# Performance work log

Measured on AMD Instinct MI355X. Metric: run time of the kernel, lower is better.

## Reference

```python
import jax, jax.numpy as jnp
import numpy as np

BSZ = 4
SL = 4096
NPAD = 8192  # next power of two >= 2*SL (preconvolve)
K = 16       # num_eigh
D = 128      # n_embd
KU = 3       # k_u
NM = 2       # num_models (residual boosting)
NL = 2       # n_layers per SpectralSSM
DIN = 64     # vocab / d_in
DOUT = 64    # d_out
HID = 512    # scale * n_embd
EPS = 1e-6


def _top_eigh(sl, k):
    # Hankel matrix Z[i,j] = 2 / ((i+j)^3 - (i+j)), 1-indexed
    idx = np.arange(1, sl + 1, dtype=np.float64)
    s = idx[:, None] + idx[None, :]
    Z = 2.0 / (s ** 3 - s)
    w, v = np.linalg.eigh(Z)
    return np.abs(w[-k:]).astype(np.float32), v[:, -k:].astype(np.float32)


def setup_inputs() -> dict:
    key = jax.random.key(0)
    ks = jax.random.split(key, 12)
    sigma_np, phi_np = _top_eigh(SL, K)
    mx = DOUT ** (-0.5)
    std = 0.02
    return {
        "inputs": jax.random.randint(ks[0], (BSZ, SL), 0, DIN),
        "targets": jax.random.randint(ks[1], (BSZ, SL), 0, DOUT),
        "sigma": jnp.asarray(sigma_np),
        "phi": jnp.asarray(phi_np),
        "embed_w": std * jax.random.normal(ks[2], (NM, DIN, D), jnp.float32),
        "rn_w": jnp.ones((NM, NL, D), jnp.float32),
        "M_u": jax.random.uniform(ks[3], (NM, NL, KU, D, D), jnp.float32, -mx, mx),
        "M_phi_plus": std * jax.random.normal(ks[4], (NM, NL, K, D, D), jnp.float32),
        "M_phi_minus": std * jax.random.normal(ks[5], (NM, NL, K, D, D), jnp.float32),
        "fc1_w": std * jax.random.normal(ks[6], (NM, NL, 2 * HID, D), jnp.float32),
        "fc2_w": std * jax.random.normal(ks[7], (NM, NL, D, HID), jnp.float32),
        "out_w": std * jax.random.normal(ks[8], (NM, DOUT, D), jnp.float32),
    }


def _rms(x, w):
    return x * jax.lax.rsqrt(jnp.mean(x * x, axis=-1, keepdims=True) + EPS) * w


def _mlp(x, w1, w2):
    h = x @ w1.T                      # (b, s, 2*HID)
    y, gate = h[..., :HID], h[..., HID:]
    return (y * jax.nn.silu(gate)) @ w2.T


def _stu(x, V, alt, Mp, Mm, Mu):
    # spectral FFT long convolution with K eigenfilters
    U = jnp.fft.rfft(x, n=NPAD, axis=1)                                   # (b, F, d)
    Up = jnp.fft.irfft(V[None, :, :, None] * U[:, :, None, :], n=NPAD, axis=1)[:, :SL]  # (b, s, K, d)
    Ua = jnp.fft.rfft(x * alt[None, :, None], n=NPAD, axis=1)
    Um = jnp.fft.irfft(V[None, :, :, None] * Ua[:, :, None, :], n=NPAD, axis=1)[:, :SL]
    y = jnp.einsum('bski,kio->bso', Up, Mp) + jnp.einsum('bski,kio->bso', Um, Mm)
    ar = jnp.einsum('bsd,do->bso', x, Mu[0])
    for i in range(1, KU):
        xs = jnp.pad(x, ((0, 0), (i, 0), (0, 0)))[:, :SL]
        ar = ar + jnp.einsum('bsd,do->bso', xs, Mu[i])
    return y + ar


def reference(inputs, targets, sigma, phi, embed_w, rn_w, M_u, M_phi_plus,
              M_phi_minus, fc1_w, fc2_w, out_w):
    phi_s = phi * sigma[None, :] ** 0.25                 # fold sigma^{1/4} into filters
    V = jnp.fft.rfft(phi_s, n=NPAD, axis=0)              # (F, K), preconvolve
    alt = ((-1.0) ** jnp.arange(SL)).astype(phi.dtype)

    residual = jax.nn.one_hot(targets, DOUT, dtype=phi.dtype)
    total = None
    for m in range(NM):
        x = embed_w[m][inputs]                           # (b, s, d)
        for l in range(NL):
            z = x
            x = x + _stu(_rms(x, rn_w[m, l]), V, alt,
                         M_phi_plus[m, l], M_phi_minus[m, l], M_u[m, l])
            x = x + _mlp(x, fc1_w[m, l], fc2_w[m, l])
            x = x + z
        logits = x @ out_w[m].T                          # (b, s, DOUT)
        total = logits if total is None else total + logits
        residual = residual - jax.lax.stop_gradient(logits)  # boosting target for next model
    return total
```

## Files before the change

kernel.cpp:

```cpp
#include <hip/hip_runtime.h>
#include <hip/hip_bf16.h>
#include <cstdint>

typedef unsigned short u16;
typedef __attribute__((ext_vector_type(8))) short bf16x8;
typedef __attribute__((ext_vector_type(4))) float f32x4;

#define N_ROWS 16384

__device__ __forceinline__ float bf2f(u16 u){ union{unsigned i; float f;} v; v.i = ((unsigned)u)<<16; return v.f; }
__device__ __forceinline__ u16 f2bf(float f){ union{float f; unsigned i;} v; v.f = f; unsigned r = v.i + 0x7fffu + ((v.i>>16)&1u); return (u16)(r>>16); }

__device__ __forceinline__ void gl2lds(const u16* g, u16* l){
  __builtin_amdgcn_global_load_lds((const __attribute__((address_space(1))) void*)g,
                                   (__attribute__((address_space(3))) void*)l, 16, 0, 0);
}


__global__ __launch_bounds__(256) void buildT_k(const float* __restrict__ phi, const float* __restrict__ sigma,
                                                u16* __restrict__ T){
  int idx = blockIdx.x*256 + threadIdx.x;
  int t2 = idx & 63;
  int tt = (idx>>6) & 127;
  int o  = (idx>>13) & 31;
  int k  = idx>>18;
  float sp = powf(sigma[k], 0.25f);
  int d0 = o*128 + tt - t2*2;
  float v0 = (d0   >= 0) ? phi[(size_t)d0*16 + k]*sp     : 0.f;
  float v1 = (d0-1 >= 0) ? phi[(size_t)(d0-1)*16 + k]*sp : 0.f;
  ushort2 u; u.x = f2bf(v0); u.y = f2bf(v1);
  ((ushort2*)T)[idx] = u;
}

__global__ __launch_bounds__(256) void castw_k(const float* __restrict__ Mp, const float* __restrict__ Mm,
                                               u16* __restrict__ W){
  int z = blockIdx.z; int ml = z>>5, k = (z>>1)&15, pm = z&1;
  const float* src = (pm ? Mm : Mp) + (size_t)(ml*16 + k)*16384;
  u16* dst = W + (size_t)ml*(2048*256) + (size_t)(k*128)*256 + pm*128;
  __shared__ float t[32][33];
  int ty = threadIdx.x>>5, tx = threadIdx.x&31;
  int i0 = blockIdx.x*32, o0 = blockIdx.y*32;
#pragma unroll
  for (int j=0;j<4;++j) t[ty+j*8][tx] = src[(size_t)(i0+ty+j*8)*128 + o0+tx];
  __syncthreads();
#pragma unroll
  for (int j=0;j<4;++j){
    int o = o0 + ty + j*8, i = i0 + tx;
    dst[(size_t)o*256 + i] = f2bf(t[tx][ty+j*8]);
  }
}

__global__ __launch_bounds__(256) void castmu_k(const float* __restrict__ Mu, u16* __restrict__ MuT){
  int z = blockIdx.z; int ml = z/3, j = z%3;
  const float* src = Mu + (size_t)(ml*3 + j)*16384;
  u16* dst = MuT + (size_t)ml*(128*384) + j*128;
  __shared__ float t[32][33];
  int ty = threadIdx.x>>5, tx = threadIdx.x&31;
  int i0 = blockIdx.x*32, o0 = blockIdx.y*32;
#pragma unroll
  for (int jj=0;jj<4;++jj) t[ty+jj*8][tx] = src[(size_t)(i0+ty+jj*8)*128 + o0+tx];
  __syncthreads();
#pragma unroll
  for (int jj=0;jj<4;++jj){
    int o = o0 + ty + jj*8, i = i0 + tx;
    dst[(size_t)o*384 + i] = f2bf(t[tx][ty+jj*8]);
  }
}

__global__ __launch_bounds__(256) void castf_k(const float* __restrict__ src, u16* __restrict__ dst, int n4){
  int i = blockIdx.x*256 + threadIdx.x;
  if (i < n4){
    float4 v = ((const float4*)src)[i];
    ushort4 u; u.x=f2bf(v.x); u.y=f2bf(v.y); u.z=f2bf(v.z); u.w=f2bf(v.w);
    ((ushort4*)dst)[i] = u;
  }
}


__global__ __launch_bounds__(256) void embed_k(const int* __restrict__ tok, const float* __restrict__ E,
                                               float* __restrict__ x){
  int idx = blockIdx.x*256 + threadIdx.x;
  int r = idx>>5, q = idx&31;
  int t = tok[r];
  ((float4*)(x + (size_t)r*128))[q] = ((const float4*)(E + (size_t)t*128))[q];
}

__global__ __launch_bounds__(256) void rms_k(const float* __restrict__ x, const float* __restrict__ w,
                                             u16* __restrict__ Xcat){
  int wave = threadIdx.x>>6, lane = threadIdx.x&63;
  int r = blockIdx.x*4 + wave;
  float2 xv = ((const float2*)(x + (size_t)r*128))[lane];
  float ss = xv.x*xv.x + xv.y*xv.y;
  for (int off=32; off; off>>=1) ss += __shfl_xor(ss, off, 64);
  float sc = rsqrtf(ss*(1.f/128.f) + 1e-6f);
  float2 wv = ((const float2*)w)[lane];
  float a = xv.x*sc*wv.x, b = xv.y*sc*wv.y;
  int s = r & 4095;
  float sg = (s & 1) ? -1.f : 1.f;
  ushort2* row = (ushort2*)(Xcat + (size_t)r*256);
  ushort2 u0; u0.x = f2bf(a);    u0.y = f2bf(b);
  ushort2 u1; u1.x = f2bf(a*sg); u1.y = f2bf(b*sg);
  row[lane]      = u0;
  row[64 + lane] = u1;
}

__global__ __launch_bounds__(256) void xar_k(const u16* __restrict__ Xcat, u16* __restrict__ Xar){
  int idx = blockIdx.x*256 + threadIdx.x;
  int r = idx>>5, q4 = idx&31;
  int s = r & 4095;
  ushort4 z; z.x=0; z.y=0; z.z=0; z.w=0;
#pragma unroll
  for (int j=0;j<3;++j){
    ushort4 v = (s >= j) ? ((const ushort4*)Xcat)[(size_t)(r-j)*64 + q4] : z;
    ((ushort4*)Xar)[(size_t)r*96 + j*32 + q4] = v;
  }
}

__global__ __launch_bounds__(256) void mid_k(const float* __restrict__ x, const float* __restrict__ Y,
                                             const u16* __restrict__ Yp, float* __restrict__ xmid,
                                             u16* __restrict__ xmbf){
  size_t idx = (size_t)blockIdx.x*256 + threadIdx.x;
  float4 xv = ((const float4*)x)[idx];
  float4 a  = ((const float4*)Y)[idx];
  const size_t P = (size_t)N_ROWS*32;
#pragma unroll
  for (int g=0; g<16; ++g){
    ushort4 v = ((const ushort4*)Yp)[idx + (size_t)g*P];
    a.x += bf2f(v.x); a.y += bf2f(v.y); a.z += bf2f(v.z); a.w += bf2f(v.w);
  }
  float4 r; r.x = xv.x+a.x; r.y = xv.y+a.y; r.z = xv.z+a.z; r.w = xv.w+a.w;
  ((float4*)xmid)[idx] = r;
  ushort4 u; u.x=f2bf(r.x); u.y=f2bf(r.y); u.z=f2bf(r.z); u.w=f2bf(r.w);
  ((ushort4*)xmbf)[idx] = u;
}

__global__ __launch_bounds__(256) void gate_k(const u16* __restrict__ h, u16* __restrict__ hg){
  size_t idx = (size_t)blockIdx.x*256 + threadIdx.x;
  size_t r = idx>>7, c = idx&127;
  ushort4 yv = ((const ushort4*)(h + r*1024))[c];
  ushort4 gv = ((const ushort4*)(h + r*1024 + 512))[c];
  float g0=bf2f(gv.x), g1=bf2f(gv.y), g2=bf2f(gv.z), g3=bf2f(gv.w);
  float s0 = g0/(1.f+expf(-g0)), s1 = g1/(1.f+expf(-g1)), s2 = g2/(1.f+expf(-g2)), s3 = g3/(1.f+expf(-g3));
  ushort4 o;
  o.x = f2bf(bf2f(yv.x)*s0); o.y = f2bf(bf2f(yv.y)*s1);
  o.z = f2bf(bf2f(yv.z)*s2); o.w = f2bf(bf2f(yv.w)*s3);
  ((ushort4*)(hg + r*512))[c] = o;
}

__global__ __launch_bounds__(256) void logits_k(const float* __restrict__ x, const u16* __restrict__ Wt,
                                                float* __restrict__ out, int accum){
  __shared__ u16 lw[64*130];
  for (int i = threadIdx.x; i < 8192; i += 256) lw[(i>>7)*130 + (i&127)] = Wt[i];
  __syncthreads();
  int wave = threadIdx.x>>6, lane = threadIdx.x&63;
  int r = blockIdx.x*4 + wave;
  const float* xr = x + (size_t)r*128;
  float acc = 0.f;
#pragma unroll
  for (int i=0;i<128;i+=4){
    float4 xv = *(const float4*)&xr[i];
    acc += xv.x*bf2f(lw[lane*130+i  ]) + xv.y*bf2f(lw[lane*130+i+1])
         + xv.z*bf2f(lw[lane*130+i+2]) + xv.w*bf2f(lw[lane*130+i+3]);
  }
  size_t o = (size_t)r*64 + lane;
  out[o] = accum ? (out[o] + acc) : acc;
}

template<int EPI>
__global__ __launch_bounds__(256) void gemm_k(const u16* __restrict__ A, int lda,
    const u16* __restrict__ Bt, int ldb, int Kdim, int ldc,
    u16* __restrict__ obf, float* __restrict__ of32,
    const float* __restrict__ e1, float* __restrict__ e2)
{
  __shared__ u16 Al[128*64];
  __shared__ u16 Bl[128*64];
  const int tid = threadIdx.x, w = tid>>6, lane = tid&63;
  const int wr = w>>1, wc = w&1;
  const int r0 = blockIdx.x*128, c0 = blockIdx.y*128;
  const int ccs = (((lane&7) ^ (lane>>3)))*8;
  f32x4 acc[4][4] = {};
  for (int k0 = 0; k0 < Kdim; k0 += 64){
#pragma unroll
    for (int i=0;i<4;++i){
      const int rr = w*32 + i*8 + (lane>>3);
      gl2lds(A  + (size_t)(r0+rr)*lda + k0 + ccs, &Al[(w*32+i*8)*64]);
      gl2lds(Bt + (size_t)(c0+rr)*ldb + k0 + ccs, &Bl[(w*32+i*8)*64]);
    }
    __syncthreads();
#pragma unroll
    for (int ks=0; ks<2; ++ks){
      const int rc = (((ks*4 + (lane>>4)) ^ (lane&7)))*8;
      bf16x8 av[4], bv[4];
#pragma unroll
      for (int mi=0;mi<4;++mi) av[mi] = *(const bf16x8*)&Al[(wr*64+mi*16+(lane&15))*64 + rc];
#pragma unroll
      for (int ni=0;ni<4;++ni) bv[ni] = *(const bf16x8*)&Bl[(wc*64+ni*16+(lane&15))*64 + rc];
#pragma unroll
      for (int mi=0;mi<4;++mi)
#pragma unroll
        for (int ni=0;ni<4;++ni)
          acc[mi][ni] = __builtin_amdgcn_mfma_f32_16x16x32_bf16(av[mi], bv[ni], acc[mi][ni], 0,0,0);
    }
    __syncthreads();
  }
  const int lr = (lane>>4)*4, lc = lane&15;
#pragma unroll
  for (int mi=0;mi<4;++mi){
#pragma unroll
    for (int ni=0;ni<4;++ni){
      const int gr = r0 + wr*64 + mi*16 + lr;
      const int gc = c0 + wc*64 + ni*16 + lc;
      if (EPI == 0){
#pragma unroll
        for (int j=0;j<4;++j) of32[(size_t)(gr+j)*ldc + gc] = acc[mi][ni][j];
      } else if (EPI == 1){
#pragma unroll
        for (int j=0;j<4;++j) obf[(size_t)(gr+j)*ldc + gc] = f2bf(acc[mi][ni][j]);
      } else if (EPI == 2){
        ushort4 u; u.x=f2bf(acc[mi][ni][0]); u.y=f2bf(acc[mi][ni][1]);
                   u.z=f2bf(acc[mi][ni][2]); u.w=f2bf(acc[mi][ni][3]);
        const int bb = gr>>12, tau = gr&4095;
        *(ushort4*)&obf[((size_t)(bb*2048 + gc))*4096 + tau] = u;
      } else {
#pragma unroll
        for (int j=0;j<4;++j){ const size_t id = (size_t)(gr+j)*ldc + gc; e2[id] = acc[mi][ni][j] + e1[id] + e2[id]; }
      }
    }
  }
}

__global__ __launch_bounds__(256) void timemix_k(const u16* __restrict__ T, const u16* __restrict__ G,
                                                 u16* __restrict__ Yp)
{
  __shared__ u16 Al[128*64];
  __shared__ u16 Bl[128*64];
  const int bid = blockIdx.x;
  const int k  = bid & 15;
  const int b  = (bid>>4) & 3;
  const int qq = bid>>6;
  const int tid = threadIdx.x, w = tid>>6, lane = tid&63;
  const int wr = w>>1, wc = w&1;
  const int ccs = (((lane&7) ^ (lane>>3)))*8;
  const u16* Tk = T + (size_t)k*32*16384;
  const u16* Gk = G + ((size_t)(b*2048 + k*128))*4096;
  u16* o = Yp + (size_t)k*((size_t)N_ROWS*128) + (size_t)b*4096*128;
  const int lr = (lane>>4)*4, lc = lane&15;
  for (int qi = 0; qi < 2; ++qi){
    const int q = qi ? (31-qq) : qq;
    f32x4 acc[4][4] = {};
    for (int p = 0; p <= q; ++p){
      const u16* Ab = Tk + (size_t)(q-p)*16384;
      const u16* Bb = Gk + (size_t)p*128;
#pragma unroll
      for (int hh=0; hh<2; ++hh){
        const int k0 = hh*64;
#pragma unroll
        for (int i=0;i<4;++i){
          const int rr = w*32 + i*8 + (lane>>3);
          gl2lds(Ab + (size_t)rr*128  + k0 + ccs, &Al[(w*32+i*8)*64]);
          gl2lds(Bb + (size_t)rr*4096 + k0 + ccs, &Bl[(w*32+i*8)*64]);
        }
        __syncthreads();
#pragma unroll
        for (int ks=0; ks<2; ++ks){
          const int rc = (((ks*4 + (lane>>4)) ^ (lane&7)))*8;
          bf16x8 av[4], bv[4];
#pragma unroll
          for (int mi=0;mi<4;++mi) av[mi] = *(const bf16x8*)&Al[(wr*64+mi*16+(lane&15))*64 + rc];
#pragma unroll
          for (int ni=0;ni<4;++ni) bv[ni] = *(const bf16x8*)&Bl[(wc*64+ni*16+(lane&15))*64 + rc];
#pragma unroll
          for (int mi=0;mi<4;++mi)
#pragma unroll
            for (int ni=0;ni<4;++ni)
              acc[mi][ni] = __builtin_amdgcn_mfma_f32_16x16x32_bf16(av[mi], bv[ni], acc[mi][ni], 0,0,0);
        }
        __syncthreads();
      }
    }
#pragma unroll
    for (int mi=0;mi<4;++mi){
#pragma unroll
      for (int ni=0;ni<4;++ni){
        const int grl = q*128 + wr*64 + mi*16 + lr;
        const int gc  = wc*64 + ni*16 + lc;
#pragma unroll
        for (int j=0;j<4;++j) o[(size_t)(grl + j)*128 + gc] = f2bf(acc[mi][ni][j]);
      }
    }
  }
}

extern "C" void kernel_launch(void* const* d_in, const int* in_sizes, int n_in,
                              void* d_out, int out_size, void* d_ws, size_t ws_size,
                              hipStream_t stream)
{
  const int*   inputs = (const int*)d_in[0];
  const float* sigma  = (const float*)d_in[2];
  const float* phi    = (const float*)d_in[3];
  const float* embed  = (const float*)d_in[4];
  const float* rnw    = (const float*)d_in[5];
  const float* Mu     = (const float*)d_in[6];
  const float* Mp     = (const float*)d_in[7];
  const float* Mm     = (const float*)d_in[8];
  const float* fc1    = (const float*)d_in[9];
  const float* fc2    = (const float*)d_in[10];
  const float* outw   = (const float*)d_in[11];
  float* out = (float*)d_out;
  char* ws = (char*)d_ws;
  size_t off = 0;
  auto alloc = [&](size_t b){ size_t o = off; off += (b + 255) & ~(size_t)255; return o; };
  u16*   T    = (u16*)  (ws + alloc((size_t)16*32*16384*2));
  u16*   Wcat = (u16*)  (ws + alloc((size_t)4*2048*256*2));
  u16*   MuT  = (u16*)  (ws + alloc((size_t)4*128*384*2));
  u16*   f1T  = (u16*)  (ws + alloc((size_t)524288*2));
  u16*   f2T  = (u16*)  (ws + alloc((size_t)262144*2));
  u16*   owT  = (u16*)  (ws + alloc((size_t)16384*2));
  float* x    = (float*)(ws + alloc((size_t)N_ROWS*128*4));
  float* Y    = (float*)(ws + alloc((size_t)N_ROWS*128*4));
  u16*   Ypb  = (u16*)  (ws + alloc((size_t)16*N_ROWS*128*2));
  float* xmid = (float*)(ws + alloc((size_t)N_ROWS*128*4));
  u16*   xmbf = (u16*)  (ws + alloc((size_t)N_ROWS*128*2));
  u16*   big  = (u16*)  (ws + alloc((size_t)N_ROWS*2048*2));
  u16*   Xar  = Ypb;
  u16*   Xcat = Ypb + (size_t)N_ROWS*384;
  u16*   Gt = big;
  u16*   h  = big;
  u16*   hg = big + (size_t)N_ROWS*1024;

  buildT_k <<<16384, 256, 0, stream>>>(phi, sigma, T);
  castw_k  <<<dim3(4,4,128), 256, 0, stream>>>(Mp, Mm, Wcat);
  castmu_k <<<dim3(4,4,12),  256, 0, stream>>>(Mu, MuT);
  castf_k  <<<512, 256, 0, stream>>>(fc1,  f1T, 131072);
  castf_k  <<<256, 256, 0, stream>>>(fc2,  f2T, 65536);
  castf_k  <<<16,  256, 0, stream>>>(outw, owT, 4096);

  for (int m = 0; m < 2; ++m){
    embed_k<<<2048, 256, 0, stream>>>(inputs, embed + (size_t)m*8192, x);
    for (int l = 0; l < 2; ++l){
      const int ml = m*2 + l;
      rms_k<<<4096, 256, 0, stream>>>(x, rnw + ml*128, Xcat);
      xar_k<<<2048, 256, 0, stream>>>(Xcat, Xar);
      gemm_k<0><<<dim3(128,1), 256, 0, stream>>>(Xar, 384, MuT + (size_t)ml*128*384, 384, 384, 128,
                                                 nullptr, Y, nullptr, nullptr);
      gemm_k<2><<<dim3(128,16), 256, 0, stream>>>(Xcat, 256, Wcat + (size_t)ml*2048*256, 256, 256, 0,
                                                  Gt, nullptr, nullptr, nullptr);
      timemix_k<<<1024, 256, 0, stream>>>(T, Gt, Ypb);
      mid_k<<<2048, 256, 0, stream>>>(x, Y, Ypb, xmid, xmbf);
      gemm_k<1><<<dim3(128,8), 256, 0, stream>>>(xmbf, 128, f1T + (size_t)ml*1024*128, 128, 128, 1024,
                                                 h, nullptr, nullptr, nullptr);
      gate_k<<<8192, 256, 0, stream>>>(h, hg);
      gemm_k<3><<<dim3(128,1), 256, 0, stream>>>(hg, 512, f2T + (size_t)ml*128*512, 512, 512, 128,
                                                 nullptr, nullptr, xmid, x);
    }
    logits_k<<<4096, 256, 0, stream>>>(x, owT + (size_t)m*8192, out, m);
  }
}
```

Before: 1.250 ms.

## Restructure timemix into 256-row tiles with triple-buffered async LDS pipeline

The Toeplitz time-mixing GEMM now uses 512-thread blocks computing 256-row output tiles, with each block accumulating two eigenfilters into one partial output. This halves the partial buffers that mid_k must sum. The T matrix gains an extra zero-padded diagonal block so that 256-row tiles can index it uniformly. The inner loop uses a three-stage LDS ring with direct global-to-LDS loads, explicit vmcnt waits, raw barriers and setprio around the MFMAs, so that loads overlap compute. The cost is more LDS per block, fewer blocks, and fragile hand-placed waits.

```diff
diff --git a/kernel.cpp b/kernel.cpp
--- a/kernel.cpp
+++ b/kernel.cpp
@@ -22,10 +22,11 @@
   int idx = blockIdx.x*256 + threadIdx.x;
   int t2 = idx & 63;
   int tt = (idx>>6) & 127;
-  int o  = (idx>>13) & 31;
-  int k  = idx>>18;
+  unsigned rest = ((unsigned)idx)>>13;
+  int k  = rest / 33u;
+  int oi = rest - 33u*k;
   float sp = powf(sigma[k], 0.25f);
-  int d0 = o*128 + tt - t2*2;
+  int d0 = (oi-1)*128 + tt - t2*2;
   float v0 = (d0   >= 0) ? phi[(size_t)d0*16 + k]*sp     : 0.f;
   float v1 = (d0-1 >= 0) ? phi[(size_t)(d0-1)*16 + k]*sp : 0.f;
   ushort2 u; u.x = f2bf(v0); u.y = f2bf(v1);
@@ -124,7 +125,7 @@
   float4 a  = ((const float4*)Y)[idx];
   const size_t P = (size_t)N_ROWS*32;
 #pragma unroll
-  for (int g=0; g<16; ++g){
+  for (int g=0; g<8; ++g){
     ushort4 v = ((const ushort4*)Yp)[idx + (size_t)g*P];
     a.x += bf2f(v.x); a.y += bf2f(v.y); a.z += bf2f(v.z); a.w += bf2f(v.w);
   }
@@ -229,63 +230,110 @@
   }
 }
 
-__global__ __launch_bounds__(256) void timemix_k(const u16* __restrict__ T, const u16* __restrict__ G,
-                                                 u16* __restrict__ Yp)
+__global__ __launch_bounds__(512, 2) void timemix_k(const u16* __restrict__ T, const u16* __restrict__ G,
+                                                    u16* __restrict__ Yp)
 {
-  __shared__ u16 Al[128*64];
-  __shared__ u16 Bl[128*64];
+  __shared__ u16 Al[3][256*64];
+  __shared__ u16 Bl[3][128*64];
   const int bid = blockIdx.x;
-  const int k  = bid & 15;
-  const int b  = (bid>>4) & 3;
-  const int qq = bid>>6;
+  const int kg = bid & 7;
+  const int b  = (bid>>3) & 3;
+  const int pj = bid>>5;
   const int tid = threadIdx.x, w = tid>>6, lane = tid&63;
   const int wr = w>>1, wc = w&1;
-  const int ccs = (((lane&7) ^ (lane>>3)))*8;
-  const u16* Tk = T + (size_t)k*32*16384;
-  const u16* Gk = G + ((size_t)(b*2048 + k*128))*4096;
-  u16* o = Yp + (size_t)k*((size_t)N_ROWS*128) + (size_t)b*4096*128;
+  const int l8 = lane>>3;
+  const int ccs = ((lane&7) ^ l8)*8;
+  const int fr = lane&15;
+  const int frx = lane&7;
   const int lr = (lane>>4)*4, lc = lane&15;
-  for (int qi = 0; qi < 2; ++qi){
-    const int q = qi ? (31-qq) : qq;
+  const int rc0 = (((lane>>4)    ) ^ frx)*8;
+  const int rc1 = (((lane>>4) + 4) ^ frx)*8;
+  u16* oYp = Yp + (size_t)kg*((size_t)N_ROWS*128) + (size_t)b*4096*128;
+
+  for (int sp = 0; sp < 2; ++sp){
+    const int jq = sp ? (15-pj) : pj;
+    const int NT = 4*jq + 4;
+    const int TT = 2*NT;
+
+    auto stage = [&](int t, int part, int sbuf){
+      int tk = t, kk = kg*2;
+      if (tk >= NT){ tk -= NT; kk++; }
+      const int p = tk>>1, k0 = (tk&1)*64;
+      const u16* Tk = T + (size_t)kk*33*16384;
+      const u16* Gk = G + ((size_t)(b*2048 + kk*128))*4096 + (size_t)p*128 + k0 + ccs;
+      u16* Ab = Al[sbuf]; u16* Bb = Bl[sbuf];
+#pragma unroll
+      for (int i = part*2; i < part*2+2; ++i){
+        const int rr = w*32 + i*8;
+        const int offI = 2*jq + (rr>>7) - p + 1;
+        gl2lds(Tk + (size_t)offI*16384 + (size_t)((rr&127)+l8)*128 + k0 + ccs, &Ab[rr*64]);
+      }
+      const int ro = w*16 + part*8;
+      gl2lds(Gk + (size_t)(ro+l8)*4096, &Bb[ro*64]);
+    };
+
+    stage(0,0,0); stage(0,1,0);
+    stage(1,0,1); stage(1,1,1);
+    asm volatile("s_waitcnt vmcnt(6)");
+    __builtin_amdgcn_s_barrier();
+
     f32x4 acc[4][4] = {};
-    for (int p = 0; p <= q; ++p){
-      const u16* Ab = Tk + (size_t)(q-p)*16384;
-      const u16* Bb = Gk + (size_t)p*128;
-#pragma unroll
-      for (int hh=0; hh<2; ++hh){
-        const int k0 = hh*64;
-#pragma unroll
-        for (int i=0;i<4;++i){
-          const int rr = w*32 + i*8 + (lane>>3);
-          gl2lds(Ab + (size_t)rr*128  + k0 + ccs, &Al[(w*32+i*8)*64]);
-          gl2lds(Bb + (size_t)rr*4096 + k0 + ccs, &Bl[(w*32+i*8)*64]);
+    int cur = 0;
+    for (int t = 0; t < TT; ++t){
+      const int sbuf = (cur+2 >= 3) ? cur-1 : cur+2;
+      const u16* Ab = Al[cur]; const u16* Bb = Bl[cur];
+      {
+        bf16x8 av[4], bv[4];
+#pragma unroll
+        for (int mi=0;mi<4;++mi) av[mi] = *(const bf16x8*)&Ab[(wr*64+mi*16+fr)*64 + rc0];
+#pragma unroll
+        for (int ni=0;ni<4;++ni) bv[ni] = *(const bf16x8*)&Bb[(wc*64+ni*16+fr)*64 + rc0];
+        if (t+2 < TT) stage(t+2, 0, sbuf);
+        __builtin_amdgcn_s_barrier();
+        asm volatile("s_waitcnt lgkmcnt(0)");
+        __builtin_amdgcn_sched_barrier(0);
+        __builtin_amdgcn_s_setprio(1);
+#pragma unroll
+        for (int mi=0;mi<4;++mi)
+#pragma unroll
+          for (int ni=0;ni<4;++ni)
+            acc[mi][ni] = __builtin_amdgcn_mfma_f32_16x16x32_bf16(av[mi], bv[ni], acc[mi][ni], 0,0,0);
+        __builtin_amdgcn_s_setprio(0);
+        __builtin_amdgcn_s_barrier();
+      }
+      {
+        bf16x8 av[4], bv[4];
+#pragma unroll
+        for (int mi=0;mi<4;++mi) av[mi] = *(const bf16x8*)&Ab[(wr*64+mi*16+fr)*64 + rc1];
+#pragma unroll
+        for (int ni=0;ni<4;++ni) bv[ni] = *(const bf16x8*)&Bb[(wc*64+ni*16+fr)*64 + rc1];
+        if (t+2 < TT) stage(t+2, 1, sbuf);
+        __builtin_amdgcn_s_barrier();
+        asm volatile("s_waitcnt lgkmcnt(0)");
+        __builtin_amdgcn_sched_barrier(0);
+        __builtin_amdgcn_s_setprio(1);
+#pragma unroll
+        for (int mi=0;mi<4;++mi)
+#pragma unroll
+          for (int ni=0;ni<4;++ni)
+            acc[mi][ni] = __builtin_amdgcn_mfma_f32_16x16x32_bf16(av[mi], bv[ni], acc[mi][ni], 0,0,0);
+        __builtin_amdgcn_s_setprio(0);
+        if (t+1 < TT){
+          if (t+2 < TT) asm volatile("s_waitcnt vmcnt(6)");
+          else          asm volatile("s_waitcnt vmcnt(0)");
         }
-        __syncthreads();
-#pragma unroll
-        for (int ks=0; ks<2; ++ks){
-          const int rc = (((ks*4 + (lane>>4)) ^ (lane&7)))*8;
-          bf16x8 av[4], bv[4];
-#pragma unroll
-          for (int mi=0;mi<4;++mi) av[mi] = *(const bf16x8*)&Al[(wr*64+mi*16+(lane&15))*64 + rc];
-#pragma unroll
-          for (int ni=0;ni<4;++ni) bv[ni] = *(const bf16x8*)&Bl[(wc*64+ni*16+(lane&15))*64 + rc];
-#pragma unroll
-          for (int mi=0;mi<4;++mi)
-#pragma unroll
-            for (int ni=0;ni<4;++ni)
-              acc[mi][ni] = __builtin_amdgcn_mfma_f32_16x16x32_bf16(av[mi], bv[ni], acc[mi][ni], 0,0,0);
-        }
-        __syncthreads();
+        __builtin_amdgcn_s_barrier();
       }
+      cur = (cur==2) ? 0 : cur+1;
     }
 #pragma unroll
     for (int mi=0;mi<4;++mi){
 #pragma unroll
       for (int ni=0;ni<4;++ni){
-        const int grl = q*128 + wr*64 + mi*16 + lr;
+        const int grl = jq*256 + wr*64 + mi*16 + lr;
         const int gc  = wc*64 + ni*16 + lc;
 #pragma unroll
-        for (int j=0;j<4;++j) o[(size_t)(grl + j)*128 + gc] = f2bf(acc[mi][ni][j]);
+        for (int j=0;j<4;++j) oYp[(size_t)(grl + j)*128 + gc] = f2bf(acc[mi][ni][j]);
       }
     }
   }
@@ -309,8 +357,8 @@
   float* out = (float*)d_out;
   char* ws = (char*)d_ws;
   size_t off = 0;
-  auto alloc = [&](size_t b){ size_t o = off; off += (b + 255) & ~(size_t)255; return o; };
-  u16*   T    = (u16*)  (ws + alloc((size_t)16*32*16384*2));
+  auto alloc = [&](size_t bytes){ size_t o = off; off += (bytes + 255) & ~(size_t)255; return o; };
+  u16*   T    = (u16*)  (ws + alloc((size_t)16*33*16384*2));
   u16*   Wcat = (u16*)  (ws + alloc((size_t)4*2048*256*2));
   u16*   MuT  = (u16*)  (ws + alloc((size_t)4*128*384*2));
   u16*   f1T  = (u16*)  (ws + alloc((size_t)524288*2));
@@ -318,7 +366,7 @@
   u16*   owT  = (u16*)  (ws + alloc((size_t)16384*2));
   float* x    = (float*)(ws + alloc((size_t)N_ROWS*128*4));
   float* Y    = (float*)(ws + alloc((size_t)N_ROWS*128*4));
-  u16*   Ypb  = (u16*)  (ws + alloc((size_t)16*N_ROWS*128*2));
+  u16*   Ypb  = (u16*)  (ws + alloc((size_t)8*N_ROWS*128*2));
   float* xmid = (float*)(ws + alloc((size_t)N_ROWS*128*4));
   u16*   xmbf = (u16*)  (ws + alloc((size_t)N_ROWS*128*2));
   u16*   big  = (u16*)  (ws + alloc((size_t)N_ROWS*2048*2));
@@ -328,7 +376,7 @@
   u16*   h  = big;
   u16*   hg = big + (size_t)N_ROWS*1024;
 
-  buildT_k <<<16384, 256, 0, stream>>>(phi, sigma, T);
+  buildT_k <<<16896, 256, 0, stream>>>(phi, sigma, T);
   castw_k  <<<dim3(4,4,128), 256, 0, stream>>>(Mp, Mm, Wcat);
   castmu_k <<<dim3(4,4,12),  256, 0, stream>>>(Mu, MuT);
   castf_k  <<<512, 256, 0, stream>>>(fc1,  f1T, 131072);
@@ -345,7 +393,7 @@
                                                  nullptr, Y, nullptr, nullptr);
       gemm_k<2><<<dim3(128,16), 256, 0, stream>>>(Xcat, 256, Wcat + (size_t)ml*2048*256, 256, 256, 0,
                                                   Gt, nullptr, nullptr, nullptr);
-      timemix_k<<<1024, 256, 0, stream>>>(T, Gt, Ypb);
+      timemix_k<<<256, 512, 0, stream>>>(T, Gt, Ypb);
       mid_k<<<2048, 256, 0, stream>>>(x, Y, Ypb, xmid, xmbf);
       gemm_k<1><<<dim3(128,8), 256, 0, stream>>>(xmbf, 128, f1T + (size_t)ml*1024*128, 128, 128, 1024,
                                                  h, nullptr, nullptr, nullptr);
```

Measured after the change: 1.289 ms. 3.1% more time.

## Fuse shift into RMS, gate into fc1 GEMM, add 64-row GEMM, transpose Gt layout

Applied to the files above, without the earlier changes.

The rms kernel now scatters the shifted autoregressive copies directly into Xar, so the separate xar kernel is gone. The SiLU gate is fused into a new fc1 GEMM epilogue that pairs the y and gate columns per block and exchanges them through LDS, which removes the h buffer round trip. A 64-row GEMM variant doubles the block count for the N=128 projections (Mu and fc2) to improve occupancy. The spectral projection now computes Gt as a swapped-operand GEMM with a plain bf16 store, writing it in a [channel][b*4096+tau] layout that timemix reads with a new stride.

```diff
diff --git a/kernel.cpp b/kernel.cpp
--- a/kernel.cpp
+++ b/kernel.cpp
@@ -86,7 +86,7 @@
 }
 
 __global__ __launch_bounds__(256) void rms_k(const float* __restrict__ x, const float* __restrict__ w,
-                                             u16* __restrict__ Xcat){
+                                             u16* __restrict__ Xcat, u16* __restrict__ Xar){
   int wave = threadIdx.x>>6, lane = threadIdx.x&63;
   int r = blockIdx.x*4 + wave;
   float2 xv = ((const float2*)(x + (size_t)r*128))[lane];
@@ -102,17 +102,11 @@
   ushort2 u1; u1.x = f2bf(a*sg); u1.y = f2bf(b*sg);
   row[lane]      = u0;
   row[64 + lane] = u1;
-}
-
-__global__ __launch_bounds__(256) void xar_k(const u16* __restrict__ Xcat, u16* __restrict__ Xar){
-  int idx = blockIdx.x*256 + threadIdx.x;
-  int r = idx>>5, q4 = idx&31;
-  int s = r & 4095;
-  ushort4 z; z.x=0; z.y=0; z.z=0; z.w=0;
+  ushort2 z2; z2.x = 0; z2.y = 0;
 #pragma unroll
   for (int j=0;j<3;++j){
-    ushort4 v = (s >= j) ? ((const ushort4*)Xcat)[(size_t)(r-j)*64 + q4] : z;
-    ((ushort4*)Xar)[(size_t)r*96 + j*32 + q4] = v;
+    if (s + j < 4096) ((ushort2*)(Xar + (size_t)(r+j)*384 + j*128))[lane] = u0;
+    if (s < j)        ((ushort2*)(Xar + (size_t)r*384     + j*128))[lane] = z2;
   }
 }
 
@@ -132,19 +126,6 @@
   ((float4*)xmid)[idx] = r;
   ushort4 u; u.x=f2bf(r.x); u.y=f2bf(r.y); u.z=f2bf(r.z); u.w=f2bf(r.w);
   ((ushort4*)xmbf)[idx] = u;
-}
-
-__global__ __launch_bounds__(256) void gate_k(const u16* __restrict__ h, u16* __restrict__ hg){
-  size_t idx = (size_t)blockIdx.x*256 + threadIdx.x;
-  size_t r = idx>>7, c = idx&127;
-  ushort4 yv = ((const ushort4*)(h + r*1024))[c];
-  ushort4 gv = ((const ushort4*)(h + r*1024 + 512))[c];
-  float g0=bf2f(gv.x), g1=bf2f(gv.y), g2=bf2f(gv.z), g3=bf2f(gv.w);
-  float s0 = g0/(1.f+expf(-g0)), s1 = g1/(1.f+expf(-g1)), s2 = g2/(1.f+expf(-g2)), s3 = g3/(1.f+expf(-g3));
-  ushort4 o;
-  o.x = f2bf(bf2f(yv.x)*s0); o.y = f2bf(bf2f(yv.y)*s1);
-  o.z = f2bf(bf2f(yv.z)*s2); o.w = f2bf(bf2f(yv.w)*s3);
-  ((ushort4*)(hg + r*512))[c] = o;
 }
 
 __global__ __launch_bounds__(256) void logits_k(const float* __restrict__ x, const u16* __restrict__ Wt,
@@ -210,22 +191,137 @@
     for (int ni=0;ni<4;++ni){
       const int gr = r0 + wr*64 + mi*16 + lr;
       const int gc = c0 + wc*64 + ni*16 + lc;
+      if (EPI == 1){
+#pragma unroll
+        for (int j=0;j<4;++j) obf[(size_t)(gr+j)*ldc + gc] = f2bf(acc[mi][ni][j]);
+      }
+    }
+  }
+}
+
+template<int EPI>
+__global__ __launch_bounds__(256) void gemm64_k(const u16* __restrict__ A, int lda,
+    const u16* __restrict__ Bt, int ldb, int Kdim, int ldc,
+    float* __restrict__ of32, const float* __restrict__ e1, float* __restrict__ e2)
+{
+  __shared__ u16 Al[64*64];
+  __shared__ u16 Bl[128*64];
+  const int tid = threadIdx.x, w = tid>>6, lane = tid&63;
+  const int r0 = blockIdx.x*64;
+  const int l8 = lane>>3;
+  const int ccs = (((lane&7) ^ l8))*8;
+  f32x4 acc[4][2] = {};
+  for (int k0 = 0; k0 < Kdim; k0 += 64){
+#pragma unroll
+    for (int i=0;i<2;++i){
+      const int rr = w*16 + i*8 + l8;
+      gl2lds(A + (size_t)(r0+rr)*lda + k0 + ccs, &Al[(w*16+i*8)*64]);
+    }
+#pragma unroll
+    for (int i=0;i<4;++i){
+      const int rr = w*32 + i*8 + l8;
+      gl2lds(Bt + (size_t)rr*ldb + k0 + ccs, &Bl[(w*32+i*8)*64]);
+    }
+    __syncthreads();
+#pragma unroll
+    for (int ks=0; ks<2; ++ks){
+      const int rc = (((ks*4 + (lane>>4)) ^ (lane&7)))*8;
+      bf16x8 av[4], bv[2];
+#pragma unroll
+      for (int mi=0;mi<4;++mi) av[mi] = *(const bf16x8*)&Al[(mi*16+(lane&15))*64 + rc];
+#pragma unroll
+      for (int ni=0;ni<2;++ni) bv[ni] = *(const bf16x8*)&Bl[(w*32+ni*16+(lane&15))*64 + rc];
+#pragma unroll
+      for (int mi=0;mi<4;++mi)
+#pragma unroll
+        for (int ni=0;ni<2;++ni)
+          acc[mi][ni] = __builtin_amdgcn_mfma_f32_16x16x32_bf16(av[mi], bv[ni], acc[mi][ni], 0,0,0);
+    }
+    __syncthreads();
+  }
+  const int lr = (lane>>4)*4, lc = lane&15;
+#pragma unroll
+  for (int mi=0;mi<4;++mi){
+#pragma unroll
+    for (int ni=0;ni<2;++ni){
+      const int gr = r0 + mi*16 + lr;
+      const int gc = w*32 + ni*16 + lc;
       if (EPI == 0){
 #pragma unroll
         for (int j=0;j<4;++j) of32[(size_t)(gr+j)*ldc + gc] = acc[mi][ni][j];
-      } else if (EPI == 1){
-#pragma unroll
-        for (int j=0;j<4;++j) obf[(size_t)(gr+j)*ldc + gc] = f2bf(acc[mi][ni][j]);
-      } else if (EPI == 2){
-        ushort4 u; u.x=f2bf(acc[mi][ni][0]); u.y=f2bf(acc[mi][ni][1]);
-                   u.z=f2bf(acc[mi][ni][2]); u.w=f2bf(acc[mi][ni][3]);
-        const int bb = gr>>12, tau = gr&4095;
-        *(ushort4*)&obf[((size_t)(bb*2048 + gc))*4096 + tau] = u;
       } else {
 #pragma unroll
         for (int j=0;j<4;++j){ const size_t id = (size_t)(gr+j)*ldc + gc; e2[id] = acc[mi][ni][j] + e1[id] + e2[id]; }
       }
     }
+  }
+}
+
+__global__ __launch_bounds__(256) void gemmgate_k(const u16* __restrict__ A,
+    const u16* __restrict__ f1T, u16* __restrict__ hg)
+{
+  __shared__ u16 Al[128*64];
+  __shared__ u16 Bl[128*64];
+  __shared__ u16 sg[128*68];
+  const int tid = threadIdx.x, w = tid>>6, lane = tid&63;
+  const int wr = w>>1, wc = w&1;
+  const int r0 = blockIdx.x*128, gj = blockIdx.y;
+  const int ccs = (((lane&7) ^ (lane>>3)))*8;
+  f32x4 acc[4][4] = {};
+  for (int k0 = 0; k0 < 128; k0 += 64){
+#pragma unroll
+    for (int i=0;i<4;++i){
+      const int rr = w*32 + i*8 + (lane>>3);
+      const int br = (rr < 64) ? (gj*64 + rr) : (512 + gj*64 + rr - 64);
+      gl2lds(A   + (size_t)(r0+rr)*128 + k0 + ccs, &Al[(w*32+i*8)*64]);
+      gl2lds(f1T + (size_t)br*128     + k0 + ccs, &Bl[(w*32+i*8)*64]);
+    }
+    __syncthreads();
+#pragma unroll
+    for (int ks=0; ks<2; ++ks){
+      const int rc = (((ks*4 + (lane>>4)) ^ (lane&7)))*8;
+      bf16x8 av[4], bv[4];
+#pragma unroll
+      for (int mi=0;mi<4;++mi) av[mi] = *(const bf16x8*)&Al[(wr*64+mi*16+(lane&15))*64 + rc];
+#pragma unroll
+      for (int ni=0;ni<4;++ni) bv[ni] = *(const bf16x8*)&Bl[(wc*64+ni*16+(lane&15))*64 + rc];
+#pragma unroll
+      for (int mi=0;mi<4;++mi)
+#pragma unroll
+        for (int ni=0;ni<4;++ni)
+          acc[mi][ni] = __builtin_amdgcn_mfma_f32_16x16x32_bf16(av[mi], bv[ni], acc[mi][ni], 0,0,0);
+    }
+    __syncthreads();
+  }
+  const int lr = (lane>>4)*4, lc = lane&15;
+  if (wc == 1){
+#pragma unroll
+    for (int mi=0;mi<4;++mi)
+#pragma unroll
+      for (int ni=0;ni<4;++ni){
+        const int rl = wr*64 + mi*16 + lr;
+        const int cl = ni*16 + lc;
+#pragma unroll
+        for (int j=0;j<4;++j){
+          float g = acc[mi][ni][j];
+          sg[(size_t)(rl+j)*68 + cl] = f2bf(g/(1.f+expf(-g)));
+        }
+      }
+  }
+  __syncthreads();
+  if (wc == 0){
+#pragma unroll
+    for (int mi=0;mi<4;++mi)
+#pragma unroll
+      for (int ni=0;ni<4;++ni){
+        const int rl = wr*64 + mi*16 + lr;
+        const int cl = ni*16 + lc;
+#pragma unroll
+        for (int j=0;j<4;++j){
+          float g = bf2f(sg[(size_t)(rl+j)*68 + cl]);
+          hg[(size_t)(r0+rl+j)*512 + gj*64 + cl] = f2bf(acc[mi][ni][j]*g);
+        }
+      }
   }
 }
 
@@ -242,7 +338,7 @@
   const int wr = w>>1, wc = w&1;
   const int ccs = (((lane&7) ^ (lane>>3)))*8;
   const u16* Tk = T + (size_t)k*32*16384;
-  const u16* Gk = G + ((size_t)(b*2048 + k*128))*4096;
+  const u16* Gk = G + (size_t)(k*128)*16384 + b*4096;
   u16* o = Yp + (size_t)k*((size_t)N_ROWS*128) + (size_t)b*4096*128;
   const int lr = (lane>>4)*4, lc = lane&15;
   for (int qi = 0; qi < 2; ++qi){
@@ -257,8 +353,8 @@
 #pragma unroll
         for (int i=0;i<4;++i){
           const int rr = w*32 + i*8 + (lane>>3);
-          gl2lds(Ab + (size_t)rr*128  + k0 + ccs, &Al[(w*32+i*8)*64]);
-          gl2lds(Bb + (size_t)rr*4096 + k0 + ccs, &Bl[(w*32+i*8)*64]);
+          gl2lds(Ab + (size_t)rr*128   + k0 + ccs, &Al[(w*32+i*8)*64]);
+          gl2lds(Bb + (size_t)rr*16384 + k0 + ccs, &Bl[(w*32+i*8)*64]);
         }
         __syncthreads();
 #pragma unroll
@@ -309,7 +405,7 @@
   float* out = (float*)d_out;
   char* ws = (char*)d_ws;
   size_t off = 0;
-  auto alloc = [&](size_t b){ size_t o = off; off += (b + 255) & ~(size_t)255; return o; };
+  auto alloc = [&](size_t bytes){ size_t o = off; off += (bytes + 255) & ~(size_t)255; return o; };
   u16*   T    = (u16*)  (ws + alloc((size_t)16*32*16384*2));
   u16*   Wcat = (u16*)  (ws + alloc((size_t)4*2048*256*2));
   u16*   MuT  = (u16*)  (ws + alloc((size_t)4*128*384*2));
@@ -321,12 +417,11 @@
   u16*   Ypb  = (u16*)  (ws + alloc((size_t)16*N_ROWS*128*2));
   float* xmid = (float*)(ws + alloc((size_t)N_ROWS*128*4));
   u16*   xmbf = (u16*)  (ws + alloc((size_t)N_ROWS*128*2));
-  u16*   big  = (u16*)  (ws + alloc((size_t)N_ROWS*2048*2));
+  u16*   big  = (u16*)  (ws + alloc((size_t)2048*16384*2));
   u16*   Xar  = Ypb;
   u16*   Xcat = Ypb + (size_t)N_ROWS*384;
   u16*   Gt = big;
-  u16*   h  = big;
-  u16*   hg = big + (size_t)N_ROWS*1024;
+  u16*   hg = big;
 
   buildT_k <<<16384, 256, 0, stream>>>(phi, sigma, T);
   castw_k  <<<dim3(4,4,128), 256, 0, stream>>>(Mp, Mm, Wcat);
@@ -339,19 +434,16 @@
     embed_k<<<2048, 256, 0, stream>>>(inputs, embed + (size_t)m*8192, x);
     for (int l = 0; l < 2; ++l){
       const int ml = m*2 + l;
-      rms_k<<<4096, 256, 0, stream>>>(x, rnw + ml*128, Xcat);
-      xar_k<<<2048, 256, 0, stream>>>(Xcat, Xar);
-      gemm_k<0><<<dim3(128,1), 256, 0, stream>>>(Xar, 384, MuT + (size_t)ml*128*384, 384, 384, 128,
-                                                 nullptr, Y, nullptr, nullptr);
-      gemm_k<2><<<dim3(128,16), 256, 0, stream>>>(Xcat, 256, Wcat + (size_t)ml*2048*256, 256, 256, 0,
+      rms_k<<<4096, 256, 0, stream>>>(x, rnw + ml*128, Xcat, Xar);
+      gemm64_k<0><<<dim3(256,1), 256, 0, stream>>>(Xar, 384, MuT + (size_t)ml*128*384, 384, 384, 128,
+                                                   Y, nullptr, nullptr);
+      gemm_k<1><<<dim3(16,128), 256, 0, stream>>>(Wcat + (size_t)ml*2048*256, 256, Xcat, 256, 256, 16384,
                                                   Gt, nullptr, nullptr, nullptr);
       timemix_k<<<1024, 256, 0, stream>>>(T, Gt, Ypb);
       mid_k<<<2048, 256, 0, stream>>>(x, Y, Ypb, xmid, xmbf);
-      gemm_k<1><<<dim3(128,8), 256, 0, stream>>>(xmbf, 128, f1T + (size_t)ml*1024*128, 128, 128, 1024,
-                                                 h, nullptr, nullptr, nullptr);
-      gate_k<<<8192, 256, 0, stream>>>(h, hg);
-      gemm_k<3><<<dim3(128,1), 256, 0, stream>>>(hg, 512, f2T + (size_t)ml*128*512, 512, 512, 128,
-                                                 nullptr, nullptr, xmid, x);
+      gemmgate_k<<<dim3(128,8), 256, 0, stream>>>(xmbf, f1T + (size_t)ml*1024*128, hg);
+      gemm64_k<3><<<dim3(256,1), 256, 0, stream>>>(hg, 512, f2T + (size_t)ml*128*512, 512, 512, 128,
+                                                   nullptr, xmid, x);
     }
     logits_k<<<4096, 256, 0, stream>>>(x, owT + (size_t)m*8192, out, m);
   }
```

Result: faster. 1.108 ms (-11.4%).
